# Kernel optimization log

Measured on AMD Instinct MI355X. Metric: run time of the kernel, lower is better.

## Reference

```python
import jax, jax.numpy as jnp
import numpy as np

NUM_HEADS = 8
QUERY_HEAD_DIM = 32
POS_HEAD_DIM = 4
EMBED_DIM = 512
POS_DIM = 192
SEQ_LEN = 1024
BATCH = 8
IN_PROJ_DIM = (QUERY_HEAD_DIM * 2 + POS_HEAD_DIM) * NUM_HEADS  # 544


def setup_inputs() -> dict:
    key = jax.random.key(0)
    k1, k2, k3, k4, k5 = jax.random.split(key, 5)
    x = jax.random.normal(k1, (SEQ_LEN, BATCH, EMBED_DIM), dtype=jnp.float32)
    pos_emb = jax.random.normal(k2, (1, 2 * SEQ_LEN - 1, POS_DIM), dtype=jnp.float32)
    key_padding_mask = jnp.zeros((BATCH, SEQ_LEN), dtype=bool)
    # in_proj: ScaledLinear(embed_dim -> in_proj_dim) with initial_scale qhd**-0.25
    scale_in = QUERY_HEAD_DIM ** (-0.25) / np.sqrt(EMBED_DIM)
    W_in = jax.random.normal(k3, (EMBED_DIM, IN_PROJ_DIM), dtype=jnp.float32) * scale_in
    b_in = jax.random.normal(k4, (IN_PROJ_DIM,), dtype=jnp.float32) * 0.01
    # linear_pos: ScaledLinear(pos_dim -> num_heads*pos_head_dim), no bias, scale 0.05
    W_pos = jax.random.normal(k5, (POS_DIM, NUM_HEADS * POS_HEAD_DIM), dtype=jnp.float32) * (0.05 / np.sqrt(POS_DIM))
    return {"x": x, "pos_emb": pos_emb, "W_in": W_in, "b_in": b_in,
            "W_pos": W_pos, "key_padding_mask": key_padding_mask}


def reference(x, pos_emb, W_in, b_in, W_pos, key_padding_mask):
    S, B, _ = x.shape
    H, QH, PH = NUM_HEADS, QUERY_HEAD_DIM, POS_HEAD_DIM
    qd = H * QH
    xp = x @ W_in + b_in                          # (S, B, in_proj_dim)
    q = xp[..., :qd].reshape(S, B, H, QH)
    k = xp[..., qd:2 * qd].reshape(S, B, H, QH)   # Whiten/Balancer are identity in eval
    p = xp[..., 2 * qd:].reshape(S, B, H, PH)
    # content scores: (H, B, T, Sk)
    attn_scores = jnp.einsum('tbhd,sbhd->hbts', q, k)
    # positional scores
    pe = (pos_emb @ W_pos).reshape(2 * S - 1, H, PH)          # (2S-1, H, PH)
    pos_scores = jnp.einsum('tbhd,nhd->hbtn', p, pe)          # (H, B, T, 2S-1)
    # relative shift: out[h,b,t,j] = pos_scores[h,b,t, (S-1) - t + j]
    idx = (S - 1) - jnp.arange(S)[:, None] + jnp.arange(S)[None, :]  # (S, S)
    shifted = jnp.take_along_axis(pos_scores, idx[None, None, :, :], axis=-1)
    attn_scores = attn_scores + shifted
    # key padding mask: True positions get -1000 (as in masked_fill)
    attn_scores = jnp.where(key_padding_mask[None, :, None, :], -1000.0, attn_scores)
    return jax.nn.softmax(attn_scores, axis=-1)  # (H, B, T, S)
```

## Files before the change

### kernel.cpp

```cpp
#include <hip/hip_runtime.h>

#define SEQ  1024
#define BATCH 8
#define NH   8
#define EMB  512
#define QHD  32
#define PHD  4
#define PDIM 192
#define NPROJ 544
#define NPE  2047
#define TBLK 64

typedef float nf4 __attribute__((ext_vector_type(4)));
typedef short bf16x8 __attribute__((ext_vector_type(8)));
typedef float f32x4 __attribute__((ext_vector_type(4)));

__device__ __forceinline__ unsigned short f2bf_rne(float f) {
    unsigned int u = __float_as_uint(f);
    unsigned int r = (u + 0x7fffu + ((u >> 16) & 1u)) >> 16;
    return (unsigned short)r;
}
__device__ __forceinline__ float bf2f(unsigned short b) {
    return __uint_as_float(((unsigned int)b) << 16);
}

__global__ __launch_bounds__(256) void convx_kernel(const float* __restrict__ x,
                                                    unsigned short* __restrict__ xhi,
                                                    unsigned short* __restrict__ xlo) {
    int i = (blockIdx.x * 256 + threadIdx.x) * 8;
    float4 a = *(const float4*)(x + i);
    float4 b = *(const float4*)(x + i + 4);
    ushort4 h0, l0, h1, l1;
    h0.x = f2bf_rne(a.x); l0.x = f2bf_rne(a.x - bf2f(h0.x));
    h0.y = f2bf_rne(a.y); l0.y = f2bf_rne(a.y - bf2f(h0.y));
    h0.z = f2bf_rne(a.z); l0.z = f2bf_rne(a.z - bf2f(h0.z));
    h0.w = f2bf_rne(a.w); l0.w = f2bf_rne(a.w - bf2f(h0.w));
    h1.x = f2bf_rne(b.x); l1.x = f2bf_rne(b.x - bf2f(h1.x));
    h1.y = f2bf_rne(b.y); l1.y = f2bf_rne(b.y - bf2f(h1.y));
    h1.z = f2bf_rne(b.z); l1.z = f2bf_rne(b.z - bf2f(h1.z));
    h1.w = f2bf_rne(b.w); l1.w = f2bf_rne(b.w - bf2f(h1.w));
    *(ushort4*)(xhi + i) = h0; *(ushort4*)(xhi + i + 4) = h1;
    *(ushort4*)(xlo + i) = l0; *(ushort4*)(xlo + i + 4) = l1;
}

__global__ __launch_bounds__(256) void convw_kernel(const float* __restrict__ W,
                                                    unsigned short* __restrict__ whT,
                                                    unsigned short* __restrict__ wlT) {
    __shared__ float tile[32][33];
    const int n0 = blockIdx.x * 32, k0 = blockIdx.y * 32;
    const int c = threadIdx.x & 31, r0 = threadIdx.x >> 5;
#pragma unroll
    for (int i = 0; i < 4; ++i) {
        int r = r0 + i * 8;
        tile[r][c] = W[(size_t)(k0 + r) * NPROJ + n0 + c];
    }
    __syncthreads();
#pragma unroll
    for (int i = 0; i < 4; ++i) {
        int n = r0 + i * 8;
        float v = tile[c][n];
        unsigned short h = f2bf_rne(v);
        unsigned short l = f2bf_rne(v - bf2f(h));
        whT[(size_t)(n0 + n) * 512 + k0 + c] = h;
        wlT[(size_t)(n0 + n) * 512 + k0 + c] = l;
    }
}

__global__ __launch_bounds__(256) void pe_kernel(const float* __restrict__ pos_emb,
                                                 const float* __restrict__ W_pos,
                                                 float* __restrict__ pe_g) {
    int n  = blockIdx.x * 64 + (threadIdx.x & 63);
    int hd = blockIdx.y * 4 + (threadIdx.x >> 6);
    if (n >= NPE) return;
    const float* pr = pos_emb + (size_t)n * PDIM;
    float acc = 0.f;
    for (int c = 0; c < PDIM; c += 4) {
        float4 pv = *(const float4*)(pr + c);
        acc += pv.x * W_pos[(c + 0) * 32 + hd];
        acc += pv.y * W_pos[(c + 1) * 32 + hd];
        acc += pv.z * W_pos[(c + 2) * 32 + hd];
        acc += pv.w * W_pos[(c + 3) * 32 + hd];
    }
    pe_g[hd * NPE + n] = acc;
}

__global__ __launch_bounds__(256) void inproj_kernel(const unsigned short* __restrict__ xhi,
                                                     const unsigned short* __restrict__ xlo,
                                                     const unsigned short* __restrict__ whT,
                                                     const unsigned short* __restrict__ wlT,
                                                     const float* __restrict__ bias,
                                                     unsigned short* __restrict__ qhi,
                                                     unsigned short* __restrict__ qlo,
                                                     unsigned short* __restrict__ khi,
                                                     unsigned short* __restrict__ klo,
                                                     float* __restrict__ pws) {
    __shared__ __align__(16) unsigned short xh_l[8][128][8];
    __shared__ __align__(16) unsigned short xl_l[8][128][8];
    __shared__ __align__(16) unsigned short wh_l[8][32][8];
    __shared__ __align__(16) unsigned short wl_l[8][32][8];

    const int tid = threadIdx.x, lane = tid & 63, w = tid >> 6;
    const int la = lane & 15, lb = lane >> 4;
    const int m0 = blockIdx.x * 128, n0 = blockIdx.y * 32;

    const int mx = tid >> 1, k8x = (tid & 1) * 4;
    const int nw = tid >> 3, k8w = tid & 7;

    f32x4 acc[2][2];
#pragma unroll
    for (int mt = 0; mt < 2; ++mt)
#pragma unroll
        for (int nt = 0; nt < 2; ++nt) acc[mt][nt] = (f32x4){0.f, 0.f, 0.f, 0.f};

    for (int step = 0; step < 8; ++step) {
        const int k0 = step * 64;
        const unsigned short* sxh = xhi + (size_t)(m0 + mx) * 512 + k0 + k8x * 8;
        const unsigned short* sxl = xlo + (size_t)(m0 + mx) * 512 + k0 + k8x * 8;
#pragma unroll
        for (int j = 0; j < 4; ++j) {
            *(uint4*)&xh_l[k8x + j][mx][0] = *(const uint4*)(sxh + j * 8);
            *(uint4*)&xl_l[k8x + j][mx][0] = *(const uint4*)(sxl + j * 8);
        }
        *(uint4*)&wh_l[k8w][nw][0] = *(const uint4*)(whT + (size_t)(n0 + nw) * 512 + k0 + k8w * 8);
        *(uint4*)&wl_l[k8w][nw][0] = *(const uint4*)(wlT + (size_t)(n0 + nw) * 512 + k0 + k8w * 8);
        __syncthreads();
#pragma unroll
        for (int ks = 0; ks < 2; ++ks) {
            bf16x8 bh[2], bl[2], ah[2], al[2];
#pragma unroll
            for (int mt = 0; mt < 2; ++mt) {
                bh[mt] = *(const bf16x8*)&xh_l[ks * 4 + lb][w * 32 + mt * 16 + la][0];
                bl[mt] = *(const bf16x8*)&xl_l[ks * 4 + lb][w * 32 + mt * 16 + la][0];
            }
#pragma unroll
            for (int nt = 0; nt < 2; ++nt) {
                ah[nt] = *(const bf16x8*)&wh_l[ks * 4 + lb][nt * 16 + la][0];
                al[nt] = *(const bf16x8*)&wl_l[ks * 4 + lb][nt * 16 + la][0];
            }
#pragma unroll
            for (int mt = 0; mt < 2; ++mt)
#pragma unroll
                for (int nt = 0; nt < 2; ++nt) {
                    acc[mt][nt] = __builtin_amdgcn_mfma_f32_16x16x32_bf16(ah[nt], bh[mt], acc[mt][nt], 0, 0, 0);
                    acc[mt][nt] = __builtin_amdgcn_mfma_f32_16x16x32_bf16(ah[nt], bl[mt], acc[mt][nt], 0, 0, 0);
                    acc[mt][nt] = __builtin_amdgcn_mfma_f32_16x16x32_bf16(al[nt], bh[mt], acc[mt][nt], 0, 0, 0);
                }
        }
        __syncthreads();
    }

    const int by = blockIdx.y;
#pragma unroll
    for (int mt = 0; mt < 2; ++mt) {
        const int m = m0 + w * 32 + mt * 16 + la;
        const int s = m >> 3, bb = m & 7;
#pragma unroll
        for (int nt = 0; nt < 2; ++nt) {
            const int dloc = nt * 16 + lb * 4;
            float4 b4 = *(const float4*)(bias + n0 + dloc);
            float v0 = acc[mt][nt][0] + b4.x;
            float v1 = acc[mt][nt][1] + b4.y;
            float v2 = acc[mt][nt][2] + b4.z;
            float v3 = acc[mt][nt][3] + b4.w;
            if (by < 16) {
                const int h = by & 7;
                size_t base = (((size_t)(h * 8 + bb) * SEQ + s) * 32 + dloc);
                ushort4 hi, lo;
                hi.x = f2bf_rne(v0); lo.x = f2bf_rne(v0 - bf2f(hi.x));
                hi.y = f2bf_rne(v1); lo.y = f2bf_rne(v1 - bf2f(hi.y));
                hi.z = f2bf_rne(v2); lo.z = f2bf_rne(v2 - bf2f(hi.z));
                hi.w = f2bf_rne(v3); lo.w = f2bf_rne(v3 - bf2f(hi.w));
                if (by < 8) {
                    *(ushort4*)(qhi + base) = hi;
                    *(ushort4*)(qlo + base) = lo;
                } else {
                    *(ushort4*)(khi + base) = hi;
                    *(ushort4*)(klo + base) = lo;
                }
            } else {
                const int h = nt * 4 + lb;
                float4 o; o.x = v0; o.y = v1; o.z = v2; o.w = v3;
                *(float4*)(pws + ((size_t)(h * 8 + bb) * SEQ + s) * 4) = o;
            }
        }
    }
}

__global__ __launch_bounds__(512, 1) void attn_kernel(const unsigned short* __restrict__ qhi,
                                                      const unsigned short* __restrict__ qlo,
                                                      const unsigned short* __restrict__ khi,
                                                      const unsigned short* __restrict__ klo,
                                                      const float* __restrict__ pws,
                                                      const float* __restrict__ pe_g,
                                                      const unsigned char* __restrict__ km,
                                                      float* __restrict__ out) {
    __shared__ __align__(16) unsigned short khi_lds[SEQ * 32];
    __shared__ __align__(16) unsigned short klo_lds[SEQ * 32];
    __shared__ __align__(16) float pe4_lds[1088][4];
    __shared__ float red_m[4][16][2];
    __shared__ float red_s[4][16][2];

    const int hb = blockIdx.y;
    const int h = hb >> 3, b = hb & 7;
    const int t0 = blockIdx.x * TBLK;
    const int tid = threadIdx.x, lane = tid & 63, w = tid >> 6;
    const int la = lane & 15, lb = lane >> 4;
    const int i_t = w >> 1, j_s = w & 1;

    const unsigned short* ghi = khi + (size_t)hb * (SEQ * 32);
    const unsigned short* glo = klo + (size_t)hb * (SEQ * 32);
#pragma unroll
    for (int it = 0; it < 8; ++it) {
        int idx = it * 512 + tid;
        uint4 a = *(const uint4*)(ghi + idx * 8);
        uint4 c = *(const uint4*)(glo + idx * 8);
        *(uint4*)(khi_lds + idx * 8) = a;
        *(uint4*)(klo_lds + idx * 8) = c;
    }
    const int nbase = SEQ - 1 - t0 - (TBLK - 1);
#pragma unroll
    for (int it = 0; it < 9; ++it) {
        int idx = it * 512 + tid;
        if (idx < 4 * 1088) {
            int d = idx / 1088, o = idx - d * 1088;
            float v = 0.f;
            if (o < 1087) v = pe_g[(h * 4 + d) * NPE + nbase + o];
            pe4_lds[o][d] = v;
        }
    }
    __syncthreads();

    const int t_local = i_t * 16 + la;
    const int t = t0 + t_local;
    const size_t qoff = ((size_t)hb * SEQ + t) * 32 + lb * 8;
    const bf16x8 bqh = *(const bf16x8*)(qhi + qoff);
    const bf16x8 bql = *(const bf16x8*)(qlo + qoff);

    f32x4 acc[32];
#pragma unroll
    for (int m = 0; m < 32; ++m) acc[m] = (f32x4){0.f, 0.f, 0.f, 0.f};

#pragma unroll
    for (int m = 0; m < 32; ++m) {
        const int srow = j_s * 512 + m * 16 + la;
        const bf16x8 ah = *(const bf16x8*)(khi_lds + srow * 32 + lb * 8);
        const bf16x8 al = *(const bf16x8*)(klo_lds + srow * 32 + lb * 8);
        acc[m] = __builtin_amdgcn_mfma_f32_16x16x32_bf16(ah, bqh, acc[m], 0, 0, 0);
        acc[m] = __builtin_amdgcn_mfma_f32_16x16x32_bf16(ah, bql, acc[m], 0, 0, 0);
        acc[m] = __builtin_amdgcn_mfma_f32_16x16x32_bf16(al, bqh, acc[m], 0, 0, 0);
    }

    const float4 pvv = *(const float4*)(pws + ((size_t)hb * SEQ + t) * 4);
    const int lane_off = j_s * 512 + lb * 4 + (TBLK - 1) - t_local;
#pragma unroll
    for (int m = 0; m < 32; ++m) {
        const int o = lane_off + m * 16;
#pragma unroll
        for (int j = 0; j < 4; ++j) {
            float4 e = *(const float4*)&pe4_lds[o + j][0];
            acc[m][j] += pvv.x * e.x + pvv.y * e.y + pvv.z * e.z + pvv.w * e.w;
        }
    }

    const unsigned int* kmw = (const unsigned int*)(km + b * SEQ);
#pragma unroll
    for (int m = 0; m < 32; ++m) {
        unsigned int mk = kmw[j_s * 128 + m * 4 + lb];
        if (mk & 0x000000ffu) acc[m][0] = -1000.f;
        if (mk & 0x0000ff00u) acc[m][1] = -1000.f;
        if (mk & 0x00ff0000u) acc[m][2] = -1000.f;
        if (mk & 0xff000000u) acc[m][3] = -1000.f;
    }

    float mx = -3.4e38f;
#pragma unroll
    for (int m = 0; m < 32; ++m)
        mx = fmaxf(mx, fmaxf(fmaxf(acc[m][0], acc[m][1]), fmaxf(acc[m][2], acc[m][3])));
    mx = fmaxf(mx, __shfl_xor(mx, 16, 64));
    mx = fmaxf(mx, __shfl_xor(mx, 32, 64));
    if (lane < 16) red_m[i_t][lane][j_s] = mx;
    __syncthreads();
    const float fm = fmaxf(red_m[i_t][la][0], red_m[i_t][la][1]);
    float sum = 0.f;
#pragma unroll
    for (int m = 0; m < 32; ++m) {
        acc[m][0] = __expf(acc[m][0] - fm);
        acc[m][1] = __expf(acc[m][1] - fm);
        acc[m][2] = __expf(acc[m][2] - fm);
        acc[m][3] = __expf(acc[m][3] - fm);
        sum += (acc[m][0] + acc[m][1]) + (acc[m][2] + acc[m][3]);
    }
    sum += __shfl_xor(sum, 16, 64);
    sum += __shfl_xor(sum, 32, 64);
    if (lane < 16) red_s[i_t][lane][j_s] = sum;
    __syncthreads();
    const float inv = 1.0f / (red_s[i_t][la][0] + red_s[i_t][la][1]);

    float* op = out + ((size_t)hb * SEQ + t) * SEQ;
#pragma unroll
    for (int m = 0; m < 32; ++m) {
        nf4 o;
        o.x = acc[m][0] * inv;
        o.y = acc[m][1] * inv;
        o.z = acc[m][2] * inv;
        o.w = acc[m][3] * inv;
        __builtin_nontemporal_store(o, (nf4*)(op + j_s * 512 + m * 16 + lb * 4));
    }
}

extern "C" void kernel_launch(void* const* d_in, const int* in_sizes, int n_in,
                              void* d_out, int out_size, void* d_ws, size_t ws_size,
                              hipStream_t stream) {
    const float* x       = (const float*)d_in[0];
    const float* pos_emb = (const float*)d_in[1];
    const float* W_in    = (const float*)d_in[2];
    const float* b_in    = (const float*)d_in[3];
    const float* W_pos   = (const float*)d_in[4];
    const unsigned char* km = (const unsigned char*)d_in[5];
    float* out = (float*)d_out;

    char* ws = (char*)d_ws;
    const size_t MB = 1024 * 1024;
    unsigned short* qhi = (unsigned short*)(ws);
    unsigned short* qlo = (unsigned short*)(ws + 4 * MB);
    unsigned short* khi = (unsigned short*)(ws + 8 * MB);
    unsigned short* klo = (unsigned short*)(ws + 12 * MB);
    float*          pws = (float*)(ws + 16 * MB);
    float*          peg = (float*)(ws + 17 * MB);
    unsigned short* xhi = (unsigned short*)(ws + 18 * MB);
    unsigned short* xlo = (unsigned short*)(ws + 26 * MB);
    unsigned short* whT = (unsigned short*)(ws + 34 * MB);
    unsigned short* wlT = (unsigned short*)(ws + 35 * MB);

    hipLaunchKernelGGL(convx_kernel, dim3(2048), dim3(256), 0, stream, x, xhi, xlo);
    hipLaunchKernelGGL(convw_kernel, dim3(17, 16), dim3(256), 0, stream, W_in, whT, wlT);
    hipLaunchKernelGGL(pe_kernel, dim3(32, 8), dim3(256), 0, stream, pos_emb, W_pos, peg);
    hipLaunchKernelGGL(inproj_kernel, dim3(64, 17), dim3(256), 0, stream,
                       xhi, xlo, whT, wlT, b_in, qhi, qlo, khi, klo, pws);
    hipLaunchKernelGGL(attn_kernel, dim3(SEQ / TBLK, 64), dim3(512), 0, stream,
                       qhi, qlo, khi, klo, pws, peg, km, out);
}
```

Measured before the change: 174.0 us.

## Shrink attention tiles to 16 queries, read K from global, store pos-emb as bf16

The attention kernel now processes 16 query rows per 256-thread block across 4096 blocks, instead of 64 rows per 512-thread block. K tiles are read straight from global/L2 rather than staged into 128KB of LDS, so occupancy can rise (launch bounds allow 3 blocks/CU). The positional-embedding projection is stored as packed bf16 (one 64-bit word per position) to cut LDS and global footprint. The pe kernel is reorganised so each thread computes all 4 head dims. The trade-offs are lower precision on the positional term, repeated K reads per block (4x more K traffic through cache), and a smaller block that may expose more latency.

```diff
diff --git a/kernel.cpp b/kernel.cpp
--- a/kernel.cpp
+++ b/kernel.cpp
@@ -9,7 +9,6 @@
 #define PDIM 192
 #define NPROJ 544
 #define NPE  2047
-#define TBLK 64
 
 typedef float nf4 __attribute__((ext_vector_type(4)));
 typedef short bf16x8 __attribute__((ext_vector_type(8)));
@@ -66,22 +65,26 @@
     }
 }
 
-__global__ __launch_bounds__(256) void pe_kernel(const float* __restrict__ pos_emb,
+__global__ __launch_bounds__(128) void pe_kernel(const float* __restrict__ pos_emb,
                                                  const float* __restrict__ W_pos,
-                                                 float* __restrict__ pe_g) {
-    int n  = blockIdx.x * 64 + (threadIdx.x & 63);
-    int hd = blockIdx.y * 4 + (threadIdx.x >> 6);
+                                                 unsigned short* __restrict__ peg) {
+    const int n = blockIdx.x * 128 + threadIdx.x;
+    const int h = blockIdx.y;
     if (n >= NPE) return;
     const float* pr = pos_emb + (size_t)n * PDIM;
-    float acc = 0.f;
+    float a0 = 0.f, a1 = 0.f, a2 = 0.f, a3 = 0.f;
     for (int c = 0; c < PDIM; c += 4) {
         float4 pv = *(const float4*)(pr + c);
-        acc += pv.x * W_pos[(c + 0) * 32 + hd];
-        acc += pv.y * W_pos[(c + 1) * 32 + hd];
-        acc += pv.z * W_pos[(c + 2) * 32 + hd];
-        acc += pv.w * W_pos[(c + 3) * 32 + hd];
-    }
-    pe_g[hd * NPE + n] = acc;
+#pragma unroll
+        for (int cc = 0; cc < 4; ++cc) {
+            float pvc = cc == 0 ? pv.x : cc == 1 ? pv.y : cc == 2 ? pv.z : pv.w;
+            float4 w4 = *(const float4*)(W_pos + (c + cc) * 32 + h * 4);
+            a0 += pvc * w4.x; a1 += pvc * w4.y; a2 += pvc * w4.z; a3 += pvc * w4.w;
+        }
+    }
+    ushort4 o;
+    o.x = f2bf_rne(a0); o.y = f2bf_rne(a1); o.z = f2bf_rne(a2); o.w = f2bf_rne(a3);
+    *(ushort4*)(peg + ((size_t)h * NPE + n) * 4) = o;
 }
 
 __global__ __launch_bounds__(256) void inproj_kernel(const unsigned short* __restrict__ xhi,
@@ -186,86 +189,78 @@
     }
 }
 
-__global__ __launch_bounds__(512, 1) void attn_kernel(const unsigned short* __restrict__ qhi,
+__global__ __launch_bounds__(256, 3) void attn_kernel(const unsigned short* __restrict__ qhi,
                                                       const unsigned short* __restrict__ qlo,
                                                       const unsigned short* __restrict__ khi,
                                                       const unsigned short* __restrict__ klo,
                                                       const float* __restrict__ pws,
-                                                      const float* __restrict__ pe_g,
+                                                      const unsigned short* __restrict__ peg,
                                                       const unsigned char* __restrict__ km,
                                                       float* __restrict__ out) {
-    __shared__ __align__(16) unsigned short khi_lds[SEQ * 32];
-    __shared__ __align__(16) unsigned short klo_lds[SEQ * 32];
-    __shared__ __align__(16) float pe4_lds[1088][4];
-    __shared__ float red_m[4][16][2];
-    __shared__ float red_s[4][16][2];
-
-    const int hb = blockIdx.y;
+    __shared__ unsigned long long pe_lds[1040];
+    __shared__ float red_m[16][4];
+    __shared__ float red_s[16][4];
+
+    const int bid = blockIdx.x;
+    const int hb = bid & 63;
     const int h = hb >> 3, b = hb & 7;
-    const int t0 = blockIdx.x * TBLK;
-    const int tid = threadIdx.x, lane = tid & 63, w = tid >> 6;
+    const int t0 = (bid >> 6) * 16;
+    const int tid = threadIdx.x, lane = tid & 63;
+    const int j_s = tid >> 6;
     const int la = lane & 15, lb = lane >> 4;
-    const int i_t = w >> 1, j_s = w & 1;
-
-    const unsigned short* ghi = khi + (size_t)hb * (SEQ * 32);
-    const unsigned short* glo = klo + (size_t)hb * (SEQ * 32);
-#pragma unroll
-    for (int it = 0; it < 8; ++it) {
-        int idx = it * 512 + tid;
-        uint4 a = *(const uint4*)(ghi + idx * 8);
-        uint4 c = *(const uint4*)(glo + idx * 8);
-        *(uint4*)(khi_lds + idx * 8) = a;
-        *(uint4*)(klo_lds + idx * 8) = c;
-    }
-    const int nbase = SEQ - 1 - t0 - (TBLK - 1);
-#pragma unroll
-    for (int it = 0; it < 9; ++it) {
-        int idx = it * 512 + tid;
-        if (idx < 4 * 1088) {
-            int d = idx / 1088, o = idx - d * 1088;
-            float v = 0.f;
-            if (o < 1087) v = pe_g[(h * 4 + d) * NPE + nbase + o];
-            pe4_lds[o][d] = v;
-        }
+
+    const int nbase = (SEQ - 1) - t0 - 15;
+    const unsigned long long* pegq = (const unsigned long long*)peg + (size_t)h * NPE + nbase;
+#pragma unroll
+    for (int it = 0; it < 5; ++it) {
+        int idx = it * 256 + tid;
+        if (idx < 1039) pe_lds[idx] = pegq[idx];
     }
     __syncthreads();
 
-    const int t_local = i_t * 16 + la;
-    const int t = t0 + t_local;
+    const int t = t0 + la;
     const size_t qoff = ((size_t)hb * SEQ + t) * 32 + lb * 8;
     const bf16x8 bqh = *(const bf16x8*)(qhi + qoff);
     const bf16x8 bql = *(const bf16x8*)(qlo + qoff);
 
-    f32x4 acc[32];
-#pragma unroll
-    for (int m = 0; m < 32; ++m) acc[m] = (f32x4){0.f, 0.f, 0.f, 0.f};
-
-#pragma unroll
-    for (int m = 0; m < 32; ++m) {
-        const int srow = j_s * 512 + m * 16 + la;
-        const bf16x8 ah = *(const bf16x8*)(khi_lds + srow * 32 + lb * 8);
-        const bf16x8 al = *(const bf16x8*)(klo_lds + srow * 32 + lb * 8);
+    const unsigned short* khb = khi + (size_t)hb * (SEQ * 32);
+    const unsigned short* klb = klo + (size_t)hb * (SEQ * 32);
+
+    f32x4 acc[16];
+#pragma unroll
+    for (int m = 0; m < 16; ++m) acc[m] = (f32x4){0.f, 0.f, 0.f, 0.f};
+
+#pragma unroll
+    for (int m = 0; m < 16; ++m) {
+        const int srow = j_s * 256 + m * 16 + la;
+        const bf16x8 ah = *(const bf16x8*)(khb + (size_t)srow * 32 + lb * 8);
+        const bf16x8 al = *(const bf16x8*)(klb + (size_t)srow * 32 + lb * 8);
         acc[m] = __builtin_amdgcn_mfma_f32_16x16x32_bf16(ah, bqh, acc[m], 0, 0, 0);
         acc[m] = __builtin_amdgcn_mfma_f32_16x16x32_bf16(ah, bql, acc[m], 0, 0, 0);
         acc[m] = __builtin_amdgcn_mfma_f32_16x16x32_bf16(al, bqh, acc[m], 0, 0, 0);
     }
 
     const float4 pvv = *(const float4*)(pws + ((size_t)hb * SEQ + t) * 4);
-    const int lane_off = j_s * 512 + lb * 4 + (TBLK - 1) - t_local;
-#pragma unroll
-    for (int m = 0; m < 32; ++m) {
+    const int lane_off = j_s * 256 + lb * 4 + 15 - la;
+#pragma unroll
+    for (int m = 0; m < 16; ++m) {
         const int o = lane_off + m * 16;
 #pragma unroll
         for (int j = 0; j < 4; ++j) {
-            float4 e = *(const float4*)&pe4_lds[o + j][0];
-            acc[m][j] += pvv.x * e.x + pvv.y * e.y + pvv.z * e.z + pvv.w * e.w;
+            unsigned long long v = pe_lds[o + j];
+            unsigned int w0 = (unsigned int)v, w1 = (unsigned int)(v >> 32);
+            float e0 = __uint_as_float(w0 << 16);
+            float e1 = __uint_as_float(w0 & 0xffff0000u);
+            float e2 = __uint_as_float(w1 << 16);
+            float e3 = __uint_as_float(w1 & 0xffff0000u);
+            acc[m][j] += pvv.x * e0 + pvv.y * e1 + pvv.z * e2 + pvv.w * e3;
         }
     }
 
     const unsigned int* kmw = (const unsigned int*)(km + b * SEQ);
 #pragma unroll
-    for (int m = 0; m < 32; ++m) {
-        unsigned int mk = kmw[j_s * 128 + m * 4 + lb];
+    for (int m = 0; m < 16; ++m) {
+        unsigned int mk = kmw[j_s * 64 + m * 4 + lb];
         if (mk & 0x000000ffu) acc[m][0] = -1000.f;
         if (mk & 0x0000ff00u) acc[m][1] = -1000.f;
         if (mk & 0x00ff0000u) acc[m][2] = -1000.f;
@@ -274,16 +269,17 @@
 
     float mx = -3.4e38f;
 #pragma unroll
-    for (int m = 0; m < 32; ++m)
+    for (int m = 0; m < 16; ++m)
         mx = fmaxf(mx, fmaxf(fmaxf(acc[m][0], acc[m][1]), fmaxf(acc[m][2], acc[m][3])));
     mx = fmaxf(mx, __shfl_xor(mx, 16, 64));
     mx = fmaxf(mx, __shfl_xor(mx, 32, 64));
-    if (lane < 16) red_m[i_t][lane][j_s] = mx;
+    if (lane < 16) red_m[lane][j_s] = mx;
     __syncthreads();
-    const float fm = fmaxf(red_m[i_t][la][0], red_m[i_t][la][1]);
+    const float fm = fmaxf(fmaxf(red_m[la][0], red_m[la][1]),
+                           fmaxf(red_m[la][2], red_m[la][3]));
     float sum = 0.f;
 #pragma unroll
-    for (int m = 0; m < 32; ++m) {
+    for (int m = 0; m < 16; ++m) {
         acc[m][0] = __expf(acc[m][0] - fm);
         acc[m][1] = __expf(acc[m][1] - fm);
         acc[m][2] = __expf(acc[m][2] - fm);
@@ -292,19 +288,19 @@
     }
     sum += __shfl_xor(sum, 16, 64);
     sum += __shfl_xor(sum, 32, 64);
-    if (lane < 16) red_s[i_t][lane][j_s] = sum;
+    if (lane < 16) red_s[lane][j_s] = sum;
     __syncthreads();
-    const float inv = 1.0f / (red_s[i_t][la][0] + red_s[i_t][la][1]);
+    const float inv = 1.0f / ((red_s[la][0] + red_s[la][1]) + (red_s[la][2] + red_s[la][3]));
 
     float* op = out + ((size_t)hb * SEQ + t) * SEQ;
 #pragma unroll
-    for (int m = 0; m < 32; ++m) {
+    for (int m = 0; m < 16; ++m) {
         nf4 o;
         o.x = acc[m][0] * inv;
         o.y = acc[m][1] * inv;
         o.z = acc[m][2] * inv;
         o.w = acc[m][3] * inv;
-        __builtin_nontemporal_store(o, (nf4*)(op + j_s * 512 + m * 16 + lb * 4));
+        __builtin_nontemporal_store(o, (nf4*)(op + j_s * 256 + m * 16 + lb * 4));
     }
 }
 
@@ -326,7 +322,7 @@
     unsigned short* khi = (unsigned short*)(ws + 8 * MB);
     unsigned short* klo = (unsigned short*)(ws + 12 * MB);
     float*          pws = (float*)(ws + 16 * MB);
-    float*          peg = (float*)(ws + 17 * MB);
+    unsigned short* peg = (unsigned short*)(ws + 17 * MB);
     unsigned short* xhi = (unsigned short*)(ws + 18 * MB);
     unsigned short* xlo = (unsigned short*)(ws + 26 * MB);
     unsigned short* whT = (unsigned short*)(ws + 34 * MB);
@@ -334,9 +330,9 @@
 
     hipLaunchKernelGGL(convx_kernel, dim3(2048), dim3(256), 0, stream, x, xhi, xlo);
     hipLaunchKernelGGL(convw_kernel, dim3(17, 16), dim3(256), 0, stream, W_in, whT, wlT);
-    hipLaunchKernelGGL(pe_kernel, dim3(32, 8), dim3(256), 0, stream, pos_emb, W_pos, peg);
+    hipLaunchKernelGGL(pe_kernel, dim3(16, 8), dim3(128), 0, stream, pos_emb, W_pos, peg);
     hipLaunchKernelGGL(inproj_kernel, dim3(64, 17), dim3(256), 0, stream,
                        xhi, xlo, whT, wlT, b_in, qhi, qlo, khi, klo, pws);
-    hipLaunchKernelGGL(attn_kernel, dim3(SEQ / TBLK, 64), dim3(512), 0, stream,
+    hipLaunchKernelGGL(attn_kernel, dim3(4096), dim3(256), 0, stream,
                        qhi, qlo, khi, klo, pws, peg, km, out);
 }
```

After: 160.3 us. 7.8% less time.
